# Optimization experiments

Measured on AMD Instinct MI355X. Metric: run time of the kernel, lower is better.

Reference implementation:

```python
import jax, jax.numpy as jnp
import numpy as np

K = 16                 # neighbors
CH = (64, 64, 64)      # edge-MLP channels
C_IN = 64              # input feature channels
EPS = 1e-3             # Keras BatchNormalization default epsilon


def setup_inputs() -> dict:
    key = jax.random.key(0)
    ks = jax.random.split(key, 24)
    B, N = 256, 128
    inp = {}
    inp["points"] = jax.random.normal(ks[0], (B, N, 2), jnp.float32)
    inp["features"] = jax.random.normal(ks[1], (B, N, C_IN), jnp.float32)
    ins = [2 * C_IN, CH[0], CH[1]]
    i = 2
    for l, (cin, cout) in enumerate(zip(ins, CH)):
        inp[f"w{l}"] = jax.random.normal(ks[i], (cin, cout), jnp.float32) / np.sqrt(cin).astype(np.float32); i += 1
        inp[f"g{l}"] = jnp.ones((cout,), jnp.float32)
        inp[f"b{l}"] = jnp.zeros((cout,), jnp.float32)
        inp[f"m{l}"] = 0.1 * jax.random.normal(ks[i], (cout,), jnp.float32); i += 1
        inp[f"v{l}"] = jnp.ones((cout,), jnp.float32)
    inp["wsc"] = jax.random.normal(ks[i], (C_IN, CH[-1]), jnp.float32) / np.sqrt(C_IN).astype(np.float32); i += 1
    inp["gsc"] = jnp.ones((CH[-1],), jnp.float32)
    inp["bsc"] = jnp.zeros((CH[-1],), jnp.float32)
    inp["msc"] = 0.1 * jax.random.normal(ks[i], (CH[-1],), jnp.float32)
    inp["vsc"] = jnp.ones((CH[-1],), jnp.float32)
    return inp


def _bn(x, g, b, m, v):
    # inference-mode BatchNorm over last (channel) axis
    return (x - m) * jax.lax.rsqrt(v + EPS) * g + b


def _forward(points, features, params):
    # pairwise squared distances  [B, N, N]
    r = jnp.sum(points * points, axis=-1, keepdims=True)
    d = r - 2.0 * jnp.einsum('bnd,bmd->bnm', points, points) + jnp.swapaxes(r, 1, 2)
    # k+1 nearest (incl. self), drop self  -> [B, N, K]
    _, idx = jax.lax.top_k(-d, K + 1)
    idx = idx[:, :, 1:]
    # gather neighbor features  [B, N, K, C]
    knn = jax.vmap(lambda f, i: f[i])(features, idx)
    center = features[:, :, None, :]
    # edge features: concat(center, neighbor - center)  [B, N, K, 2C]
    x = jnp.concatenate([jnp.broadcast_to(center, knn.shape), knn - center], axis=-1)
    # edge MLP: 1x1 convs == per-edge matmuls
    for (w, g, b, m, v) in params[:-1]:
        x = jax.nn.relu(_bn(jnp.einsum('bnkc,cd->bnkd', x, w), g, b, m, v))
    pooled = jnp.mean(x, axis=2)                      # [B, N, C_out]
    wsc, gsc, bsc, msc, vsc = params[-1]
    sc = _bn(features @ wsc, gsc, bsc, msc, vsc)      # shortcut 1x1 conv + BN
    return jax.nn.relu(sc + pooled)


def reference(points, features,
              w0, g0, b0, m0, v0,
              w1, g1, b1, m1, v1,
              w2, g2, b2, m2, v2,
              wsc, gsc, bsc, msc, vsc):
    params = [(w0, g0, b0, m0, v0), (w1, g1, b1, m1, v1),
              (w2, g2, b2, m2, v2), (wsc, gsc, bsc, msc, vsc)]
    return _forward(points, features, params)
```

## Files before the change

### kernel.cpp

```cpp
#include <hip/hip_runtime.h>
#include <hip/hip_bf16.h>
#include <stdint.h>


#define EPSV 1e-3f
#define ST 72

typedef __bf16 bf16x8 __attribute__((ext_vector_type(8)));
typedef float f32x4 __attribute__((ext_vector_type(4)));
union B8 { uint4 u; bf16x8 v; };

__device__ __forceinline__ unsigned f2ord(float f) {
  unsigned u = __float_as_uint(f);
  return (u & 0x80000000u) ? ~u : (u | 0x80000000u);
}
__device__ __forceinline__ unsigned short bf1(float x) {
  union { __hip_bfloat16 h; unsigned short u; } cv;
  cv.h = __float2bfloat16(x);
  return cv.u;
}
__device__ __forceinline__ unsigned pk2(float lo, float hi) {
  union { __hip_bfloat162 h; unsigned u; } cv;
  cv.h = __float22bfloat162_rn(float2{lo, hi});
  return cv.u;
}
__device__ __forceinline__ float r2of(float x, float y) {
#pragma clang fp contract(off)
  return __fadd_rn(__fmul_rn(x, x), __fmul_rn(y, y));
}
__device__ __forceinline__ float sqdist(float rn, float xn, float yn,
                                        float xc, float yc, float rc) {
#pragma clang fp contract(off)
  const float dot = __fadd_rn(__fmul_rn(xn, xc), __fmul_rn(yn, yc));
  return __fadd_rn(__fsub_rn(rn, __fmul_rn(2.0f, dot)), rc);
}

__global__ __launch_bounds__(256, 3) void fused_kernel(
    const float* __restrict__ pts, const float* __restrict__ feat,
    const float* __restrict__ w0, const float* __restrict__ g0,
    const float* __restrict__ b0, const float* __restrict__ m0,
    const float* __restrict__ v0, const float* __restrict__ w1,
    const float* __restrict__ g1, const float* __restrict__ b1,
    const float* __restrict__ m1, const float* __restrict__ v1,
    const float* __restrict__ w2, const float* __restrict__ g2,
    const float* __restrict__ b2, const float* __restrict__ m2,
    const float* __restrict__ v2, const float* __restrict__ wsc,
    const float* __restrict__ gsc, const float* __restrict__ bsc,
    const float* __restrict__ msc, const float* __restrict__ vsc,
    float* __restrict__ out) {
  __shared__ __align__(16) unsigned short w0dT[64 * ST];
  __shared__ __align__(16) unsigned short w1T[64 * ST];
  __shared__ __align__(16) char U[32768];

  unsigned short* w0cT = (unsigned short*)U;
  unsigned short* w2T = (unsigned short*)(U + 8192);
  unsigned short* wscT = (unsigned short*)(U + 16384);

  const int tid = threadIdx.x;
  const int wv = tid >> 6;
  const int lane = tid & 63;
  const int m = lane & 15;
  const int q4 = lane >> 4;

  unsigned short* CFB = (unsigned short*)(U + 24576) + wv * (16 * 64);

#pragma unroll
  for (int q = 0; q < 8; ++q) {
    const int v = tid + 256 * q;
    const int i = v >> 4;
    const int c = (v & 15) << 2;
    const float4 w = ((const float4*)w0)[v];
    float s[4];
#pragma unroll
    for (int cc = 0; cc < 4; ++cc) s[cc] = g0[c + cc] / sqrtf(v0[c + cc] + EPSV);
    if (i < 64) {
      w0cT[(c + 0) * 64 + i] = bf1(w.x * s[0]);
      w0cT[(c + 1) * 64 + i] = bf1(w.y * s[1]);
      w0cT[(c + 2) * 64 + i] = bf1(w.z * s[2]);
      w0cT[(c + 3) * 64 + i] = bf1(w.w * s[3]);
    } else {
      const int i2 = i - 64;
      w0dT[(c + 0) * ST + i2] = bf1(w.x * s[0]);
      w0dT[(c + 1) * ST + i2] = bf1(w.y * s[1]);
      w0dT[(c + 2) * ST + i2] = bf1(w.z * s[2]);
      w0dT[(c + 3) * ST + i2] = bf1(w.w * s[3]);
    }
  }
#pragma unroll
  for (int q = 0; q < 4; ++q) {
    const int v = tid + 256 * q;
    const int i = v >> 4;
    const int c = (v & 15) << 2;
    {
      const float4 w = ((const float4*)w1)[v];
#pragma unroll
      for (int cc = 0; cc < 4; ++cc) {
        const float s = g1[c + cc] / sqrtf(v1[c + cc] + EPSV);
        const float val = (cc == 0 ? w.x : cc == 1 ? w.y : cc == 2 ? w.z : w.w);
        w1T[(c + cc) * ST + i] = bf1(val * s);
      }
    }
    {
      const float4 w = ((const float4*)w2)[v];
#pragma unroll
      for (int cc = 0; cc < 4; ++cc) {
        const float s = g2[c + cc] / sqrtf(v2[c + cc] + EPSV);
        const float val = (cc == 0 ? w.x : cc == 1 ? w.y : cc == 2 ? w.z : w.w);
        w2T[(c + cc) * 64 + i] = bf1(val * s);
      }
    }
    {
      const float4 w = ((const float4*)wsc)[v];
#pragma unroll
      for (int cc = 0; cc < 4; ++cc) {
        const float s = gsc[c + cc] / sqrtf(vsc[c + cc] + EPSV);
        const float val = (cc == 0 ? w.x : cc == 1 ? w.y : cc == 2 ? w.z : w.w);
        wscT[(c + cc) * 64 + i] = bf1(val * s);
      }
    }
  }

  f32x4 o1vv[4];
#pragma unroll
  for (int nt = 0; nt < 4; ++nt)
#pragma unroll
    for (int r = 0; r < 4; ++r) {
      const int c = nt * 16 + q4 * 4 + r;
      const float s = g1[c] / sqrtf(v1[c] + EPSV);
      o1vv[nt][r] = b1[c] - m1[c] * s;
    }
  float o0s[4], o2s[4], oscs[4];
#pragma unroll
  for (int nt = 0; nt < 4; ++nt) {
    const int c = nt * 16 + m;
    o0s[nt] = b0[c] - m0[c] * (g0[c] / sqrtf(v0[c] + EPSV));
    o2s[nt] = b2[c] - m2[c] * (g2[c] / sqrtf(v2[c] + EPSV));
    oscs[nt] = bsc[c] - msc[c] * (gsc[c] / sqrtf(vsc[c] + EPSV));
  }
  __syncthreads();

  const int row0 = blockIdx.x * 32 + wv * 8;
  const int bb = row0 >> 7;
  const float* featb = feat + bb * (128 * 64);

  {
    const int r = lane >> 3, p = lane & 7;
    const float4* fr = (const float4*)(feat + (row0 + r) * 64);
    const float4 a = fr[p * 2 + 0], bq = fr[p * 2 + 1];
    uint4 u{pk2(a.x, a.y), pk2(a.z, a.w), pk2(bq.x, bq.y), pk2(bq.z, bq.w)};
    *(uint4*)&CFB[r * 64 + p * 8] = u;
    *(uint4*)&CFB[512 + lane * 8] = make_uint4(0u, 0u, 0u, 0u);
  }

  B8 w2f[4][2];
#pragma unroll
  for (int nt = 0; nt < 4; ++nt)
#pragma unroll
    for (int t = 0; t < 2; ++t)
      w2f[nt][t].u = *(const uint4*)&w2T[(nt * 16 + m) * 64 + t * 32 + q4 * 8];

  const f32x4 fzero = {0.f, 0.f, 0.f, 0.f};
  f32x4 cacc[4] = {fzero, fzero, fzero, fzero};
  f32x4 scf[4] = {fzero, fzero, fzero, fzero};
#pragma unroll
  for (int t = 0; t < 2; ++t) {
    B8 af;
    af.u = *(const uint4*)&CFB[m * 64 + t * 32 + q4 * 8];
#pragma unroll
    for (int nt = 0; nt < 4; ++nt) {
      B8 bf_;
      bf_.u = *(const uint4*)&w0cT[(nt * 16 + m) * 64 + t * 32 + q4 * 8];
      cacc[nt] = __builtin_amdgcn_mfma_f32_16x16x32_bf16(af.v, bf_.v, cacc[nt], 0, 0, 0);
      bf_.u = *(const uint4*)&wscT[(nt * 16 + m) * 64 + t * 32 + q4 * 8];
      scf[nt] = __builtin_amdgcn_mfma_f32_16x16x32_bf16(af.v, bf_.v, scf[nt], 0, 0, 0);
    }
  }
#pragma unroll
  for (int nt = 0; nt < 4; ++nt)
#pragma unroll
    for (int r = 0; r < 4; ++r) scf[nt][r] += oscs[nt];

  __syncthreads();

  char* pwb = U + wv * 8192;
  unsigned short* X = (unsigned short*)pwb;
  float* cLS = (float*)(pwb + 2304);
  unsigned char* knnL = (unsigned char*)(pwb + 2304 + 4096);

#pragma unroll
  for (int nt = 0; nt < 4; ++nt)
#pragma unroll
    for (int r = 0; r < 4; ++r)
      cLS[(q4 * 4 + r) * 64 + nt * 16 + m] = cacc[nt][r] + o0s[nt];

  {
    unsigned long long* keysW = (unsigned long long*)pwb;
    const float* pb = pts + bb * 256;
    const float xa = pb[2 * lane], ya = pb[2 * lane + 1];
    const float xb2 = pb[2 * lane + 128], yb2 = pb[2 * lane + 129];
    const float ra = r2of(xa, ya);
    const float rb = r2of(xb2, yb2);
    const int nbase = row0 & 127;
    for (int rr = 0; rr < 8; ++rr) {
      const int n = nbase + rr;
      const float xn = pb[2 * n], yn = pb[2 * n + 1];
      const float rn = r2of(xn, yn);
      const float d0 = sqdist(rn, xn, yn, xa, ya, ra);
      const float d1 = sqdist(rn, xn, yn, xb2, yb2, rb);
      const unsigned long long key0 =
          ((unsigned long long)f2ord(d0) << 32) | (unsigned)lane;
      const unsigned long long key1 =
          ((unsigned long long)f2ord(d1) << 32) | (unsigned)(lane + 64);
      keysW[lane] = key0;
      keysW[lane + 64] = key1;
      int c0 = 0, c1 = 0;
#pragma unroll 8
      for (int j = 0; j < 128; j += 2) {
        const ulonglong2 kp = *(const ulonglong2*)&keysW[j];
        c0 += (kp.x < key0); c0 += (kp.y < key0);
        c1 += (kp.x < key1); c1 += (kp.y < key1);
      }
      if (c0 >= 1 && c0 <= 16) knnL[rr * 16 + c0 - 1] = (unsigned char)lane;
      if (c1 >= 1 && c1 <= 16) knnL[rr * 16 + c1 - 1] = (unsigned char)(lane + 64);
    }
  }

  const int kk = lane >> 2, pp = lane & 3;
  int jv[8];
#pragma unroll
  for (int rr = 0; rr < 8; ++rr) jv[rr] = knnL[rr * 16 + kk];

  for (int qo = 0; qo < 2; ++qo) {
#pragma unroll
    for (int ri = 0; ri < 4; ++ri) {
      const int rr = qo * 4 + ri;
      const int row = row0 + rr;

      {
        const float4* np_ = (const float4*)(featb + jv[rr] * 64);
        const float4* cp_ = (const float4*)(feat + row * 64);
        const float4 n0 = np_[pp * 4 + 0], n1 = np_[pp * 4 + 1];
        const float4 n2 = np_[pp * 4 + 2], n3 = np_[pp * 4 + 3];
        const float4 c0 = cp_[pp * 4 + 0], c1 = cp_[pp * 4 + 1];
        const float4 c2 = cp_[pp * 4 + 2], c3 = cp_[pp * 4 + 3];
        uint4 u;
        u.x = pk2(n0.x - c0.x, n0.y - c0.y); u.y = pk2(n0.z - c0.z, n0.w - c0.w);
        u.z = pk2(n1.x - c1.x, n1.y - c1.y); u.w = pk2(n1.z - c1.z, n1.w - c1.w);
        *(uint4*)&X[kk * ST + pp * 16] = u;
        u.x = pk2(n2.x - c2.x, n2.y - c2.y); u.y = pk2(n2.z - c2.z, n2.w - c2.w);
        u.z = pk2(n3.x - c3.x, n3.y - c3.y); u.w = pk2(n3.z - c3.z, n3.w - c3.w);
        *(uint4*)&X[kk * ST + pp * 16 + 8] = u;
      }

      f32x4 acc[4];
#pragma unroll
      for (int nt = 0; nt < 4; ++nt)
        acc[nt] = *(const f32x4*)&cLS[rr * 64 + nt * 16 + q4 * 4];
#pragma unroll
      for (int t = 0; t < 2; ++t) {
        B8 bf_;
        bf_.u = *(const uint4*)&X[m * ST + t * 32 + q4 * 8];
#pragma unroll
        for (int nt = 0; nt < 4; ++nt) {
          B8 af;
          af.u = *(const uint4*)&w0dT[(nt * 16 + m) * ST + t * 32 + q4 * 8];
          acc[nt] = __builtin_amdgcn_mfma_f32_16x16x32_bf16(af.v, bf_.v, acc[nt], 0, 0, 0);
        }
      }
#pragma unroll
      for (int nt = 0; nt < 4; ++nt) {
        uint2 wq;
        wq.x = pk2(fmaxf(acc[nt][0], 0.f), fmaxf(acc[nt][1], 0.f));
        wq.y = pk2(fmaxf(acc[nt][2], 0.f), fmaxf(acc[nt][3], 0.f));
        *(uint2*)&X[m * ST + nt * 16 + q4 * 4] = wq;
      }

#pragma unroll
      for (int nt = 0; nt < 4; ++nt) acc[nt] = o1vv[nt];
#pragma unroll
      for (int t = 0; t < 2; ++t) {
        B8 bf_;
        bf_.u = *(const uint4*)&X[m * ST + t * 32 + q4 * 8];
#pragma unroll
        for (int nt = 0; nt < 4; ++nt) {
          B8 af;
          af.u = *(const uint4*)&w1T[(nt * 16 + m) * ST + t * 32 + q4 * 8];
          acc[nt] = __builtin_amdgcn_mfma_f32_16x16x32_bf16(af.v, bf_.v, acc[nt], 0, 0, 0);
        }
      }
#pragma unroll
      for (int nt = 0; nt < 4; ++nt) {
        uint2 wq;
        wq.x = pk2(fmaxf(acc[nt][0], 0.f), fmaxf(acc[nt][1], 0.f));
        wq.y = pk2(fmaxf(acc[nt][2], 0.f), fmaxf(acc[nt][3], 0.f));
        *(uint2*)&X[m * ST + nt * 16 + q4 * 4] = wq;
      }

#pragma unroll
      for (int nt = 0; nt < 4; ++nt) acc[nt] = fzero;
#pragma unroll
      for (int t = 0; t < 2; ++t) {
        B8 af;
        af.u = *(const uint4*)&X[m * ST + t * 32 + q4 * 8];
#pragma unroll
        for (int nt = 0; nt < 4; ++nt)
          acc[nt] = __builtin_amdgcn_mfma_f32_16x16x32_bf16(af.v, w2f[nt][t].v, acc[nt], 0, 0, 0);
      }

      float pool[4];
#pragma unroll
      for (int nt = 0; nt < 4; ++nt) {
        float p = fmaxf(acc[nt][0] + o2s[nt], 0.f) + fmaxf(acc[nt][1] + o2s[nt], 0.f) +
                  fmaxf(acc[nt][2] + o2s[nt], 0.f) + fmaxf(acc[nt][3] + o2s[nt], 0.f);
        p += __shfl_xor(p, 16);
        p += __shfl_xor(p, 32);
        pool[nt] = p * 0.0625f;
      }
      if (q4 == qo) {
#pragma unroll
        for (int nt = 0; nt < 4; ++nt)
          out[row * 64 + nt * 16 + m] = fmaxf(scf[nt][ri] + pool[nt], 0.f);
      }
    }
  }
}

extern "C" void kernel_launch(void* const* d_in, const int* in_sizes, int n_in,
                              void* d_out, int out_size, void* d_ws, size_t ws_size,
                              hipStream_t stream) {
  const float* pts = (const float*)d_in[0];
  const float* feat = (const float*)d_in[1];
  const float* w0 = (const float*)d_in[2];
  const float* g0 = (const float*)d_in[3];
  const float* b0 = (const float*)d_in[4];
  const float* m0 = (const float*)d_in[5];
  const float* v0 = (const float*)d_in[6];
  const float* w1 = (const float*)d_in[7];
  const float* g1 = (const float*)d_in[8];
  const float* b1 = (const float*)d_in[9];
  const float* m1 = (const float*)d_in[10];
  const float* v1 = (const float*)d_in[11];
  const float* w2 = (const float*)d_in[12];
  const float* g2 = (const float*)d_in[13];
  const float* b2 = (const float*)d_in[14];
  const float* m2 = (const float*)d_in[15];
  const float* v2 = (const float*)d_in[16];
  const float* wsc = (const float*)d_in[17];
  const float* gsc = (const float*)d_in[18];
  const float* bsc = (const float*)d_in[19];
  const float* msc = (const float*)d_in[20];
  const float* vsc = (const float*)d_in[21];
  float* out = (float*)d_out;

  fused_kernel<<<dim3(1024), dim3(256), 0, stream>>>(
      pts, feat, w0, g0, b0, m0, v0, w1, g1, b1, m1, v1, w2, g2, b2, m2, v2,
      wsc, gsc, bsc, msc, vsc, out);
}
```

Measured before the change: 208.3 us.

## Shrink shared memory for 4 blocks/CU and use shuffle-based argmin kNN selection

Cuts the union shared buffer from 32KB to 18KB by aliasing wscT with w2T (w2 fragments are loaded into registers first, then wscT is filled after a barrier), keeping center features in registers instead of an LDS staging buffer, and packing per-wave scratch tighter. Launch bounds are raised to 4 blocks per CU. The rank-counting kNN over 128 LDS keys is replaced with 17 rounds of wave-wide min reductions via shuffles and ballots, processing 4 rows at once. Adds extra barriers and serial selection rounds, and register pressure under the tighter bound may cause spills.

```diff
diff --git a/kernel.cpp b/kernel.cpp
--- a/kernel.cpp
+++ b/kernel.cpp
@@ -35,7 +35,7 @@
   return __fadd_rn(__fsub_rn(rn, __fmul_rn(2.0f, dot)), rc);
 }
 
-__global__ __launch_bounds__(256, 3) void fused_kernel(
+__global__ __launch_bounds__(256, 4) void fused_kernel(
     const float* __restrict__ pts, const float* __restrict__ feat,
     const float* __restrict__ w0, const float* __restrict__ g0,
     const float* __restrict__ b0, const float* __restrict__ m0,
@@ -50,11 +50,11 @@
     float* __restrict__ out) {
   __shared__ __align__(16) unsigned short w0dT[64 * ST];
   __shared__ __align__(16) unsigned short w1T[64 * ST];
-  __shared__ __align__(16) char U[32768];
-
-  unsigned short* w0cT = (unsigned short*)U;
-  unsigned short* w2T = (unsigned short*)(U + 8192);
-  unsigned short* wscT = (unsigned short*)(U + 16384);
+  __shared__ __align__(16) char U[18432];
+
+  unsigned short* w2T = (unsigned short*)U;
+  unsigned short* w0cT = (unsigned short*)(U + 8192);
+  unsigned short* wscT = (unsigned short*)U;
 
   const int tid = threadIdx.x;
   const int wv = tid >> 6;
@@ -62,7 +62,9 @@
   const int m = lane & 15;
   const int q4 = lane >> 4;
 
-  unsigned short* CFB = (unsigned short*)(U + 24576) + wv * (16 * 64);
+  const int row0 = blockIdx.x * 32 + wv * 8;
+  const int bb = row0 >> 7;
+  const float* featb = feat + bb * (128 * 64);
 
 #pragma unroll
   for (int q = 0; q < 8; ++q) {
@@ -109,15 +111,6 @@
         w2T[(c + cc) * 64 + i] = bf1(val * s);
       }
     }
-    {
-      const float4 w = ((const float4*)wsc)[v];
-#pragma unroll
-      for (int cc = 0; cc < 4; ++cc) {
-        const float s = gsc[c + cc] / sqrtf(vsc[c + cc] + EPSV);
-        const float val = (cc == 0 ? w.x : cc == 1 ? w.y : cc == 2 ? w.z : w.w);
-        wscT[(c + cc) * 64 + i] = bf1(val * s);
-      }
-    }
   }
 
   f32x4 o1vv[4];
@@ -137,20 +130,21 @@
     o2s[nt] = b2[c] - m2[c] * (g2[c] / sqrtf(v2[c] + EPSV));
     oscs[nt] = bsc[c] - msc[c] * (gsc[c] / sqrtf(vsc[c] + EPSV));
   }
+
+  B8 cfa[2];
+  {
+    const int rm = row0 + (m < 8 ? m : 0);
+    const float4* fr = (const float4*)(feat + rm * 64);
+#pragma unroll
+    for (int t = 0; t < 2; ++t) {
+      const float4 a = fr[t * 8 + q4 * 2];
+      const float4 b2_ = fr[t * 8 + q4 * 2 + 1];
+      cfa[t].u = make_uint4(pk2(a.x, a.y), pk2(a.z, a.w),
+                            pk2(b2_.x, b2_.y), pk2(b2_.z, b2_.w));
+    }
+  }
+
   __syncthreads();
-
-  const int row0 = blockIdx.x * 32 + wv * 8;
-  const int bb = row0 >> 7;
-  const float* featb = feat + bb * (128 * 64);
-
-  {
-    const int r = lane >> 3, p = lane & 7;
-    const float4* fr = (const float4*)(feat + (row0 + r) * 64);
-    const float4 a = fr[p * 2 + 0], bq = fr[p * 2 + 1];
-    uint4 u{pk2(a.x, a.y), pk2(a.z, a.w), pk2(bq.x, bq.y), pk2(bq.z, bq.w)};
-    *(uint4*)&CFB[r * 64 + p * 8] = u;
-    *(uint4*)&CFB[512 + lane * 8] = make_uint4(0u, 0u, 0u, 0u);
-  }
 
   B8 w2f[4][2];
 #pragma unroll
@@ -158,21 +152,36 @@
 #pragma unroll
     for (int t = 0; t < 2; ++t)
       w2f[nt][t].u = *(const uint4*)&w2T[(nt * 16 + m) * 64 + t * 32 + q4 * 8];
+
+  __syncthreads();
+
+#pragma unroll
+  for (int q = 0; q < 4; ++q) {
+    const int v = tid + 256 * q;
+    const int i = v >> 4;
+    const int c = (v & 15) << 2;
+    const float4 w = ((const float4*)wsc)[v];
+#pragma unroll
+    for (int cc = 0; cc < 4; ++cc) {
+      const float s = gsc[c + cc] / sqrtf(vsc[c + cc] + EPSV);
+      const float val = (cc == 0 ? w.x : cc == 1 ? w.y : cc == 2 ? w.z : w.w);
+      wscT[(c + cc) * 64 + i] = bf1(val * s);
+    }
+  }
+  __syncthreads();
 
   const f32x4 fzero = {0.f, 0.f, 0.f, 0.f};
   f32x4 cacc[4] = {fzero, fzero, fzero, fzero};
   f32x4 scf[4] = {fzero, fzero, fzero, fzero};
 #pragma unroll
   for (int t = 0; t < 2; ++t) {
-    B8 af;
-    af.u = *(const uint4*)&CFB[m * 64 + t * 32 + q4 * 8];
 #pragma unroll
     for (int nt = 0; nt < 4; ++nt) {
       B8 bf_;
       bf_.u = *(const uint4*)&w0cT[(nt * 16 + m) * 64 + t * 32 + q4 * 8];
-      cacc[nt] = __builtin_amdgcn_mfma_f32_16x16x32_bf16(af.v, bf_.v, cacc[nt], 0, 0, 0);
+      cacc[nt] = __builtin_amdgcn_mfma_f32_16x16x32_bf16(cfa[t].v, bf_.v, cacc[nt], 0, 0, 0);
       bf_.u = *(const uint4*)&wscT[(nt * 16 + m) * 64 + t * 32 + q4 * 8];
-      scf[nt] = __builtin_amdgcn_mfma_f32_16x16x32_bf16(af.v, bf_.v, scf[nt], 0, 0, 0);
+      scf[nt] = __builtin_amdgcn_mfma_f32_16x16x32_bf16(cfa[t].v, bf_.v, scf[nt], 0, 0, 0);
     }
   }
 #pragma unroll
@@ -182,46 +191,65 @@
 
   __syncthreads();
 
-  char* pwb = U + wv * 8192;
+  char* pwb = U + wv * 4608;
   unsigned short* X = (unsigned short*)pwb;
   float* cLS = (float*)(pwb + 2304);
-  unsigned char* knnL = (unsigned char*)(pwb + 2304 + 4096);
-
-#pragma unroll
-  for (int nt = 0; nt < 4; ++nt)
-#pragma unroll
-    for (int r = 0; r < 4; ++r)
-      cLS[(q4 * 4 + r) * 64 + nt * 16 + m] = cacc[nt][r] + o0s[nt];
+  unsigned char* knnL = (unsigned char*)(pwb + 4352);
+
+  if (q4 < 2) {
+#pragma unroll
+    for (int nt = 0; nt < 4; ++nt)
+#pragma unroll
+      for (int r = 0; r < 4; ++r)
+        cLS[(q4 * 4 + r) * 64 + nt * 16 + m] = cacc[nt][r] + o0s[nt];
+  }
 
   {
-    unsigned long long* keysW = (unsigned long long*)pwb;
     const float* pb = pts + bb * 256;
     const float xa = pb[2 * lane], ya = pb[2 * lane + 1];
     const float xb2 = pb[2 * lane + 128], yb2 = pb[2 * lane + 129];
     const float ra = r2of(xa, ya);
     const float rb = r2of(xb2, yb2);
     const int nbase = row0 & 127;
-    for (int rr = 0; rr < 8; ++rr) {
-      const int n = nbase + rr;
-      const float xn = pb[2 * n], yn = pb[2 * n + 1];
-      const float rn = r2of(xn, yn);
-      const float d0 = sqdist(rn, xn, yn, xa, ya, ra);
-      const float d1 = sqdist(rn, xn, yn, xb2, yb2, rb);
-      const unsigned long long key0 =
-          ((unsigned long long)f2ord(d0) << 32) | (unsigned)lane;
-      const unsigned long long key1 =
-          ((unsigned long long)f2ord(d1) << 32) | (unsigned)(lane + 64);
-      keysW[lane] = key0;
-      keysW[lane + 64] = key1;
-      int c0 = 0, c1 = 0;
-#pragma unroll 8
-      for (int j = 0; j < 128; j += 2) {
-        const ulonglong2 kp = *(const ulonglong2*)&keysW[j];
-        c0 += (kp.x < key0); c0 += (kp.y < key0);
-        c1 += (kp.x < key1); c1 += (kp.y < key1);
-      }
-      if (c0 >= 1 && c0 <= 16) knnL[rr * 16 + c0 - 1] = (unsigned char)lane;
-      if (c1 >= 1 && c1 <= 16) knnL[rr * 16 + c1 - 1] = (unsigned char)(lane + 64);
+#pragma unroll 1
+    for (int g = 0; g < 2; ++g) {
+      unsigned k0[4], k1[4];
+#pragma unroll
+      for (int r = 0; r < 4; ++r) {
+        const int n = nbase + g * 4 + r;
+        const float xn = pb[2 * n], yn = pb[2 * n + 1];
+        const float rn = r2of(xn, yn);
+        k0[r] = f2ord(sqdist(rn, xn, yn, xa, ya, ra));
+        k1[r] = f2ord(sqdist(rn, xn, yn, xb2, yb2, rb));
+      }
+#pragma unroll 1
+      for (int it = 0; it <= 16; ++it) {
+        unsigned mv[4];
+#pragma unroll
+        for (int r = 0; r < 4; ++r) mv[r] = k0[r] < k1[r] ? k0[r] : k1[r];
+#pragma unroll
+        for (int off = 1; off < 64; off <<= 1) {
+#pragma unroll
+          for (int r = 0; r < 4; ++r) {
+            const unsigned t = (unsigned)__shfl_xor((int)mv[r], off);
+            mv[r] = mv[r] < t ? mv[r] : t;
+          }
+        }
+#pragma unroll
+        for (int r = 0; r < 4; ++r) {
+          const unsigned long long bal0 = __ballot(k0[r] == mv[r]);
+          const unsigned long long bal1 = __ballot(k1[r] == mv[r]);
+          const bool ch0 = bal0 != 0ull;
+          const int ml = ch0 ? (__ffsll((unsigned long long)bal0) - 1)
+                             : (__ffsll((unsigned long long)bal1) - 1);
+          const int idx = ch0 ? ml : ml + 64;
+          if (it > 0 && lane == 0)
+            knnL[(g * 4 + r) * 16 + (it - 1)] = (unsigned char)idx;
+          if (lane == ml) {
+            if (ch0) k0[r] = 0xFFFFFFFFu; else k1[r] = 0xFFFFFFFFu;
+          }
+        }
+      }
     }
   }
 
```

Result: slower. 212.5 us (+2.0%).
